# Kernel tuning notes

Measured on AMD Instinct MI355X. Metric: run time of the kernel, lower is better.

The kernel has to match this reference:

```python
import jax, jax.numpy as jnp
import numpy as np

N_NODES = 50000


def setup_inputs() -> dict:
    key = jax.random.key(0)
    k1, k2, k3, k4 = jax.random.split(key, 4)
    x = jax.random.normal(k1, (N_NODES, 256), dtype=jnp.float32)
    edge_index = jax.random.randint(k2, (2, 800000), 0, N_NODES, dtype=jnp.int64)
    W1 = jax.random.normal(k3, (256, 128), dtype=jnp.float32) * (1.0 / np.sqrt(256))
    b1 = jnp.zeros((128,), dtype=jnp.float32)
    W2 = jax.random.normal(k4, (128, 16), dtype=jnp.float32) * (1.0 / np.sqrt(128))
    b2 = jnp.zeros((16,), dtype=jnp.float32)
    return {"x": x, "edge_index": edge_index, "W1": W1, "b1": b1, "W2": W2, "b2": b2}


def _gcn_norm(edge_index, num_nodes):
    # add self-loops, then symmetric normalization D^-1/2 A D^-1/2 (PyG GCNConv default)
    loop = jnp.arange(num_nodes, dtype=edge_index.dtype)
    src = jnp.concatenate([edge_index[0], loop])
    dst = jnp.concatenate([edge_index[1], loop])
    deg = jax.ops.segment_sum(jnp.ones_like(dst, dtype=jnp.float32), dst, num_segments=num_nodes)
    dinv = jnp.where(deg > 0, jax.lax.rsqrt(deg), 0.0)
    norm = dinv[src] * dinv[dst]  # [E+N]
    return src, dst, norm


def _gcn_conv(h, W, b, src, dst, norm, num_nodes):
    h = h @ W                             # linear before propagate
    msg = h[src] * norm[:, None]          # gather + edge scaling
    agg = jax.ops.segment_sum(msg, dst, num_segments=num_nodes)  # scatter-add
    return agg + b


def reference(x, edge_index, W1, b1, W2, b2):
    n = x.shape[0]
    src, dst, norm = _gcn_norm(edge_index, n)
    h = jax.nn.relu(_gcn_conv(x, W1, b1, src, dst, norm, n))
    # F.dropout(training=False) is identity in eval mode
    out = _gcn_conv(h, W2, b2, src, dst, norm, n)
    return jax.nn.log_softmax(out, axis=1)
```

## Files before the change

kernel.cpp:

```cpp
#include <hip/hip_runtime.h>
#include <hip/hip_bf16.h>
#include <math.h>


#define FIN 256
#define FH  128
#define FO  16
#define NCOPY 8

typedef unsigned int uint;
typedef unsigned short ushort;
typedef __attribute__((ext_vector_type(8))) short bf16x8;
typedef __attribute__((ext_vector_type(4))) float f32x4;

static __device__ __forceinline__ ushort f2bf(float f) {
    __hip_bfloat16 b = __float2bfloat16(f);
    return *reinterpret_cast<ushort*>(&b);
}
static __device__ __forceinline__ float bf2f(ushort u) {
    return __uint_as_float(((uint)u) << 16);
}

__global__ __launch_bounds__(256) void GCN_zerowprep_k(int* __restrict__ count8,
                                                       int total8,
                                                       const float* __restrict__ W1,
                                                       ushort* __restrict__ whT,
                                                       ushort* __restrict__ wlT,
                                                       int nZero) {
    if ((int)blockIdx.x < nZero) {
        int i = blockIdx.x * 256 + threadIdx.x;
        if (i < total8) count8[i] = 0;
    } else {
        int i = (blockIdx.x - nZero) * 256 + threadIdx.x;
        int k = i >> 7, c = i & 127;
        float w = W1[i];
        ushort hh = f2bf(w);
        ushort hl = f2bf(w - bf2f(hh));
        whT[c * 256 + k] = hh;
        wlT[c * 256 + k] = hl;
    }
}

#define G1_BR 64
#define G1_KC 32

__global__ __launch_bounds__(256, 4) void GCN_histgemm_k(
        const float* __restrict__ x, const ushort* __restrict__ whT,
        const ushort* __restrict__ wlT, ushort* __restrict__ h1,
        const int* __restrict__ edge, int* __restrict__ count8,
        int* __restrict__ rank, int N, int E, int nGemm) {
    __shared__ __align__(16) ushort xh_s[G1_BR * G1_KC];
    __shared__ __align__(16) ushort xl_s[G1_BR * G1_KC];
    __shared__ __align__(16) ushort wh_s[FH * G1_KC];
    __shared__ __align__(16) ushort wl_s[FH * G1_KC];
    int tid = threadIdx.x;

    if ((int)blockIdx.x >= nGemm) {
        int b = blockIdx.x - nGemm;
        int i = b * 256 + tid;
        if (i < E) {
            int c = b & (NCOPY - 1);
            rank[i] = atomicAdd(&count8[(size_t)c * N + edge[E + i]], 1);
        }
        return;
    }

    int row0 = blockIdx.x * G1_BR;
    int ln = tid & 63;
    int w  = tid >> 6;
    int ln15 = ln & 15;
    int q16  = ln >> 4;

    f32x4 acc[4][2];
    #pragma unroll
    for (int mr = 0; mr < 4; mr++)
        #pragma unroll
        for (int nc = 0; nc < 2; nc++) acc[mr][nc] = (f32x4){0.f, 0.f, 0.f, 0.f};

    for (int kc = 0; kc < FIN; kc += G1_KC) {
        #pragma unroll
        for (int j = 0; j < 2; j++) {
            int u = tid + j * 256;
            int r = u >> 3, kq = u & 7;
            int gr = row0 + r;
            float4 v = make_float4(0.f, 0.f, 0.f, 0.f);
            if (gr < N) v = *(const float4*)&x[(size_t)gr * FIN + kc + kq * 4];
            ushort h0 = f2bf(v.x), h1v = f2bf(v.y), h2 = f2bf(v.z), h3 = f2bf(v.w);
            ushort l0 = f2bf(v.x - bf2f(h0));
            ushort l1 = f2bf(v.y - bf2f(h1v));
            ushort l2 = f2bf(v.z - bf2f(h2));
            ushort l3 = f2bf(v.w - bf2f(h3));
            uint2 hw, lw;
            hw.x = (uint)h0 | ((uint)h1v << 16);
            hw.y = (uint)h2 | ((uint)h3 << 16);
            lw.x = (uint)l0 | ((uint)l1 << 16);
            lw.y = (uint)l2 | ((uint)l3 << 16);
            int byte = (r * 64 + kq * 8) ^ (((r >> 1) & 3) << 4);
            *(uint2*)((char*)xh_s + byte) = hw;
            *(uint2*)((char*)xl_s + byte) = lw;
        }
        #pragma unroll
        for (int j = 0; j < 2; j++) {
            int u = tid + j * 256;
            int c = u >> 2, ku = u & 3;
            uint4 vh = *(const uint4*)&whT[(size_t)c * 256 + kc + ku * 8];
            uint4 vl = *(const uint4*)&wlT[(size_t)c * 256 + kc + ku * 8];
            int byte = (c * 64 + ku * 16) ^ (((c >> 1) & 3) << 4);
            *(uint4*)((char*)wh_s + byte) = vh;
            *(uint4*)((char*)wl_s + byte) = vl;
        }
        __syncthreads();

        bf16x8 ah[4], al[4], bh[2], bl[2];
        #pragma unroll
        for (int mr = 0; mr < 4; mr++) {
            int r = mr * 16 + ln15;
            int byte = r * 64 + ((q16 * 16) ^ (((r >> 1) & 3) << 4));
            ah[mr] = *(const bf16x8*)((const char*)xh_s + byte);
            al[mr] = *(const bf16x8*)((const char*)xl_s + byte);
        }
        #pragma unroll
        for (int nc = 0; nc < 2; nc++) {
            int c = w * 32 + nc * 16 + ln15;
            int byte = c * 64 + ((q16 * 16) ^ (((c >> 1) & 3) << 4));
            bh[nc] = *(const bf16x8*)((const char*)wh_s + byte);
            bl[nc] = *(const bf16x8*)((const char*)wl_s + byte);
        }
        #pragma unroll
        for (int mr = 0; mr < 4; mr++)
            #pragma unroll
            for (int nc = 0; nc < 2; nc++) {
                acc[mr][nc] = __builtin_amdgcn_mfma_f32_16x16x32_bf16(
                    ah[mr], bh[nc], acc[mr][nc], 0, 0, 0);
                acc[mr][nc] = __builtin_amdgcn_mfma_f32_16x16x32_bf16(
                    al[mr], bh[nc], acc[mr][nc], 0, 0, 0);
                acc[mr][nc] = __builtin_amdgcn_mfma_f32_16x16x32_bf16(
                    ah[mr], bl[nc], acc[mr][nc], 0, 0, 0);
            }
        __syncthreads();
    }

    #pragma unroll
    for (int mr = 0; mr < 4; mr++) {
        #pragma unroll
        for (int nc = 0; nc < 2; nc++) {
            int cw = w * 32 + nc * 16 + ln15;
            #pragma unroll
            for (int j = 0; j < 4; j++) {
                int gr = row0 + mr * 16 + q16 * 4 + j;
                if (gr < N) h1[(size_t)gr * FH + cw] = f2bf(acc[mr][nc][j]);
            }
        }
    }
}

__global__ __launch_bounds__(256) void GCN_chpfxbsum_k(int* __restrict__ count8,
                                                       int* __restrict__ count,
                                                       int* __restrict__ bsum,
                                                       int N) {
    int tid = threadIdx.x;
    int d = blockIdx.x * 256 + tid;
    int local = 0;
    if (d < N) {
        int run = 0;
        #pragma unroll
        for (int c = 0; c < NCOPY; c++) {
            int* p = &count8[(size_t)c * N + d];
            int v = *p; *p = run; run += v;
        }
        count[d] = run;
        local = run + 1;
    }
    __shared__ int red[256];
    red[tid] = local;
    __syncthreads();
    for (int st = 128; st > 0; st >>= 1) {
        if (tid < st) red[tid] += red[tid + st];
        __syncthreads();
    }
    if (tid == 0) bsum[blockIdx.x] = red[0];
}

__global__ __launch_bounds__(256) void GCN_scan2_k(const int* __restrict__ count,
                                                   const int* __restrict__ bsum,
                                                   int2* __restrict__ rd2,
                                                   int2* __restrict__ edata, int N) {
    int tid = threadIdx.x;
    int b = blockIdx.x;
    int d = b * 256 + tid;
    int cnt1 = (d < N) ? count[d] + 1 : 0;

    __shared__ int red[256];
    int offp = 0;
    for (int t = tid; t < b; t += 256) offp += bsum[t];
    red[tid] = offp;
    __syncthreads();
    for (int st = 128; st > 0; st >>= 1) {
        if (tid < st) red[tid] += red[tid + st];
        __syncthreads();
    }
    int blockOff = red[0];
    __syncthreads();

    __shared__ int ssum[256];
    ssum[tid] = cnt1;
    __syncthreads();
    for (int off = 1; off < 256; off <<= 1) {
        int t = (tid >= off) ? ssum[tid - off] : 0;
        __syncthreads();
        ssum[tid] += t;
        __syncthreads();
    }
    int r = blockOff + ssum[tid] - cnt1;

    if (d < N) {
        float dv = rsqrtf((float)cnt1);
        rd2[d] = make_int2(r, __float_as_int(dv));
        edata[r] = make_int2(d, __float_as_int(dv * dv));
    }
    if (b == gridDim.x - 1 && tid == 255) rd2[N] = make_int2(blockOff + ssum[255], 0);
}

__global__ __launch_bounds__(256) void GCN_fill_k(const int* __restrict__ edge,
                                                  const int* __restrict__ rank,
                                                  const int* __restrict__ count8,
                                                  const int2* __restrict__ rd2,
                                                  int2* __restrict__ edata,
                                                  int N, int E) {
    int i = blockIdx.x * 256 + threadIdx.x;
    if (i >= E) return;
    int s = edge[i];
    int d = edge[E + i];
    int rk = rank[i];
    int c = (i >> 8) & (NCOPY - 1);
    int2 rdd = rd2[d];
    float ds = __int_as_float(rd2[s].y);
    int slot = rdd.x + 1 + count8[(size_t)c * N + d] + rk;
    edata[slot] = make_int2(s, __float_as_int(ds * __int_as_float(rdd.y)));
}

__global__ __launch_bounds__(256) void GCN_agg1gemm2_k(
        const ushort* __restrict__ h1, const int2* __restrict__ rd2,
        const int2* __restrict__ ed, const float* __restrict__ b1,
        const float* __restrict__ W2, ushort* __restrict__ h2b, int N) {
    __shared__ float w2s[FH][FO];
    __shared__ float hs[16][FH + 4];
    int tid = threadIdx.x;
    #pragma unroll
    for (int j = 0; j < (FH * FO) / 256; j++) {
        int i = tid + j * 256;
        w2s[i >> 4][i & 15] = W2[i];
    }

    int node0 = blockIdx.x * 16;
    int local = tid >> 4;
    int j = tid & 15;
    int node = node0 + local;

    if (node < N) {
        int beg = rd2[node].x, end = rd2[node + 1].x;
        const uint4* hp = (const uint4*)h1;

        float a[8];
        #pragma unroll
        for (int t = 0; t < 8; t++) a[t] = 0.f;

        int i = beg;
        for (; i + 4 <= end; i += 4) {
            int2 e0 = ed[i + 0], e1 = ed[i + 1], e2 = ed[i + 2], e3 = ed[i + 3];
            float w0 = __int_as_float(e0.y), w1 = __int_as_float(e1.y);
            float w2 = __int_as_float(e2.y), w3 = __int_as_float(e3.y);
            uint4 g0 = hp[(size_t)e0.x * 16 + j];
            uint4 g1 = hp[(size_t)e1.x * 16 + j];
            uint4 g2 = hp[(size_t)e2.x * 16 + j];
            uint4 g3 = hp[(size_t)e3.x * 16 + j];
            #pragma unroll
            for (int q = 0; q < 4; q++) {
                uint u0 = (&g0.x)[q], u1 = (&g1.x)[q], u2 = (&g2.x)[q], u3 = (&g3.x)[q];
                a[q*2+0] += __uint_as_float(u0 << 16) * w0;
                a[q*2+1] += __uint_as_float(u0 & 0xFFFF0000u) * w0;
                a[q*2+0] += __uint_as_float(u1 << 16) * w1;
                a[q*2+1] += __uint_as_float(u1 & 0xFFFF0000u) * w1;
                a[q*2+0] += __uint_as_float(u2 << 16) * w2;
                a[q*2+1] += __uint_as_float(u2 & 0xFFFF0000u) * w2;
                a[q*2+0] += __uint_as_float(u3 << 16) * w3;
                a[q*2+1] += __uint_as_float(u3 & 0xFFFF0000u) * w3;
            }
        }
        for (; i < end; i++) {
            int2 e = ed[i];
            float w = __int_as_float(e.y);
            uint4 g = hp[(size_t)e.x * 16 + j];
            #pragma unroll
            for (int q = 0; q < 4; q++) {
                uint u = (&g.x)[q];
                a[q*2+0] += __uint_as_float(u << 16) * w;
                a[q*2+1] += __uint_as_float(u & 0xFFFF0000u) * w;
            }
        }

        const float4* bp = (const float4*)b1;
        float4 bb0 = bp[j * 2 + 0];
        float4 bb1 = bp[j * 2 + 1];
        float4 o0, o1;
        o0.x = fmaxf(a[0] + bb0.x, 0.f);
        o0.y = fmaxf(a[1] + bb0.y, 0.f);
        o0.z = fmaxf(a[2] + bb0.z, 0.f);
        o0.w = fmaxf(a[3] + bb0.w, 0.f);
        o1.x = fmaxf(a[4] + bb1.x, 0.f);
        o1.y = fmaxf(a[5] + bb1.y, 0.f);
        o1.z = fmaxf(a[6] + bb1.z, 0.f);
        o1.w = fmaxf(a[7] + bb1.w, 0.f);
        *(float4*)&hs[local][j * 8 + 0] = o0;
        *(float4*)&hs[local][j * 8 + 4] = o1;
    }
    __syncthreads();

    float acc = 0.f;
    #pragma unroll 8
    for (int k = 0; k < FH; k++) acc += hs[local][k] * w2s[k][j];
    if (node < N) h2b[(size_t)node * FO + j] = f2bf(acc);
}

__global__ __launch_bounds__(256) void GCN_agg2_k(const ushort* __restrict__ h2b,
                                                  const int2* __restrict__ rd2,
                                                  const int2* __restrict__ ed,
                                                  const float* __restrict__ b2,
                                                  float* __restrict__ out, int N) {
    int tid = threadIdx.x;
    int node = blockIdx.x * 32 + (tid >> 3);
    if (node >= N) return;
    int f2 = tid & 7;
    int beg = rd2[node].x, end = rd2[node + 1].x;
    const uint* hp = (const uint*)h2b;
    float a0 = 0.f, a1 = 0.f;
    int i = beg;
    for (; i + 4 <= end; i += 4) {
        int2 e0 = ed[i + 0], e1 = ed[i + 1], e2 = ed[i + 2], e3 = ed[i + 3];
        uint u0 = hp[(size_t)e0.x * 8 + f2];
        uint u1 = hp[(size_t)e1.x * 8 + f2];
        uint u2 = hp[(size_t)e2.x * 8 + f2];
        uint u3 = hp[(size_t)e3.x * 8 + f2];
        float w0 = __int_as_float(e0.y), w1 = __int_as_float(e1.y);
        float w2 = __int_as_float(e2.y), w3 = __int_as_float(e3.y);
        a0 += __uint_as_float(u0 << 16) * w0 + __uint_as_float(u1 << 16) * w1
            + __uint_as_float(u2 << 16) * w2 + __uint_as_float(u3 << 16) * w3;
        a1 += __uint_as_float(u0 & 0xFFFF0000u) * w0 + __uint_as_float(u1 & 0xFFFF0000u) * w1
            + __uint_as_float(u2 & 0xFFFF0000u) * w2 + __uint_as_float(u3 & 0xFFFF0000u) * w3;
    }
    for (; i < end; i++) {
        int2 e = ed[i];
        uint u = hp[(size_t)e.x * 8 + f2];
        float w = __int_as_float(e.y);
        a0 += __uint_as_float(u << 16) * w;
        a1 += __uint_as_float(u & 0xFFFF0000u) * w;
    }
    float2 bb = ((const float2*)b2)[f2];
    float v0 = a0 + bb.x;
    float v1 = a1 + bb.y;
    float mx = fmaxf(v0, v1);
    #pragma unroll
    for (int m = 4; m >= 1; m >>= 1) mx = fmaxf(mx, __shfl_xor(mx, m, 8));
    float s = expf(v0 - mx) + expf(v1 - mx);
    #pragma unroll
    for (int m = 4; m >= 1; m >>= 1) s += __shfl_xor(s, m, 8);
    float ls = logf(s);
    float2 o = make_float2(v0 - mx - ls, v1 - mx - ls);
    ((float2*)out)[(size_t)node * 8 + f2] = o;
}

extern "C" void kernel_launch(void* const* d_in, const int* in_sizes, int n_in,
                              void* d_out, int out_size, void* d_ws, size_t ws_size,
                              hipStream_t stream) {
    (void)n_in; (void)out_size; (void)ws_size;
    const float* x  = (const float*)d_in[0];
    const int*   edp = (const int*)d_in[1];
    const float* W1 = (const float*)d_in[2];
    const float* b1 = (const float*)d_in[3];
    const float* W2 = (const float*)d_in[4];
    const float* b2 = (const float*)d_in[5];
    float* out = (float*)d_out;

    int N = in_sizes[0] / FIN;
    int E = in_sizes[1] / 2;
    int M = E + N;
    int nScanBlocks = (N + 255) / 256;

    char* p = (char*)d_ws;
    auto take = [&](size_t bytes) -> char* {
        char* r = p;
        p += (bytes + 255) & ~(size_t)255;
        return r;
    };
    int*    count  = (int*)take((size_t)N * 4);
    int*    count8 = (int*)take((size_t)NCOPY * N * 4);
    int*    rank   = (int*)take((size_t)E * 4);
    int2*   rd2    = (int2*)take((size_t)(N + 1) * 8);
    int*    bsum   = (int*)take((size_t)nScanBlocks * 4);
    int2*   edata  = (int2*)take((size_t)M * 8);
    ushort* whT    = (ushort*)take((size_t)FH * FIN * 2);
    ushort* wlT    = (ushort*)take((size_t)FH * FIN * 2);
    ushort* h1     = (ushort*)take((size_t)N * FH * 2);
    ushort* h2b    = (ushort*)take((size_t)N * FO * 2);

    int eBlocks = (E + 255) / 256;
    int nGemm   = (N + G1_BR - 1) / G1_BR;
    int total8  = NCOPY * N;
    int nZero   = (total8 + 255) / 256;

    GCN_zerowprep_k<<<nZero + (FIN * FH) / 256, 256, 0, stream>>>(
        count8, total8, W1, whT, wlT, nZero);
    GCN_histgemm_k<<<nGemm + eBlocks, 256, 0, stream>>>(
        x, whT, wlT, h1, edp, count8, rank, N, E, nGemm);
    GCN_chpfxbsum_k<<<nScanBlocks, 256, 0, stream>>>(count8, count, bsum, N);
    GCN_scan2_k<<<nScanBlocks, 256, 0, stream>>>(count, bsum, rd2, edata, N);
    GCN_fill_k<<<eBlocks, 256, 0, stream>>>(edp, rank, count8, rd2, edata, N, E);
    GCN_agg1gemm2_k<<<(N + 15) / 16, 256, 0, stream>>>(h1, rd2, edata, b1, W2, h2b, N);
    GCN_agg2_k<<<(N + 31) / 32, 256, 0, stream>>>(h2b, rd2, edata, b2, out, N);
}
```

Before: 120.6 us.

## Replace global-atomic degree histogram with LDS-privatized packed 16-bit chunk histograms

Replaces the 8-copy global atomic degree histogram with per-chunk histograms built in shared memory. Each of 64 edge chunks is handled by 2 blocks that each cover half the nodes, with two 16-bit counters packed per word. This removes global atomics and the zeroing pass, and the histogram becomes its own kernel separate from the GEMM. In exchange it adds a 64-way per-word prefix pass, only 128 histogram blocks, no overlap with the GEMM, and counters that overflow if any node gets more than 65535 edges in one chunk.

New measurement: 130.6 us. 1.08x slower.

```diff
diff --git a/kernel.cpp b/kernel.cpp
--- a/kernel.cpp
+++ b/kernel.cpp
@@ -6,7 +6,8 @@
 #define FIN 256
 #define FH  128
 #define FO  16
-#define NCOPY 8
+#define NCHUNK64 64
+#define WPR_MAX 12544
 
 typedef unsigned int uint;
 typedef unsigned short ushort;
@@ -21,49 +22,60 @@
     return __uint_as_float(((uint)u) << 16);
 }
 
-__global__ __launch_bounds__(256) void GCN_zerowprep_k(int* __restrict__ count8,
-                                                       int total8,
-                                                       const float* __restrict__ W1,
-                                                       ushort* __restrict__ whT,
-                                                       ushort* __restrict__ wlT,
-                                                       int nZero) {
-    if ((int)blockIdx.x < nZero) {
-        int i = blockIdx.x * 256 + threadIdx.x;
-        if (i < total8) count8[i] = 0;
-    } else {
-        int i = (blockIdx.x - nZero) * 256 + threadIdx.x;
-        int k = i >> 7, c = i & 127;
-        float w = W1[i];
-        ushort hh = f2bf(w);
-        ushort hl = f2bf(w - bf2f(hh));
-        whT[c * 256 + k] = hh;
-        wlT[c * 256 + k] = hl;
-    }
+__global__ __launch_bounds__(256) void GCN_wprep_k(const float* __restrict__ W1,
+                                                   ushort* __restrict__ whT,
+                                                   ushort* __restrict__ wlT) {
+    int i = blockIdx.x * 256 + threadIdx.x;
+    int k = i >> 7, c = i & 127;
+    float w = W1[i];
+    ushort hh = f2bf(w);
+    ushort hl = f2bf(w - bf2f(hh));
+    whT[c * 256 + k] = hh;
+    wlT[c * 256 + k] = hl;
+}
+
+__global__ __launch_bounds__(256) void GCN_hist_k(const int* __restrict__ edge,
+                                                  uint* __restrict__ cw,
+                                                  int* __restrict__ rank,
+                                                  int E, int ech,
+                                                  int nWords, int wpr) {
+    __shared__ uint lh[WPR_MAX];
+    int tid = threadIdx.x;
+    int r = blockIdx.x & 1;
+    int c = blockIdx.x >> 1;
+    int w0 = r * wpr;
+    int wlim = nWords - w0; if (wlim > wpr) wlim = wpr;
+    for (int j = tid; j < wlim; j += 256) lh[j] = 0;
+    __syncthreads();
+    int base = c * ech;
+    int lim = base + ech; if (lim > E) lim = E;
+    for (int i = base + tid; i < lim; i += 256) {
+        int d = edge[E + i];
+        int wd = (d >> 1) - w0;
+        if ((unsigned)wd < (unsigned)wlim) {
+            int sh = (d & 1) << 4;
+            uint old = atomicAdd(&lh[wd], 1u << sh);
+            rank[i] = (int)((old >> sh) & 0xFFFFu);
+        }
+    }
+    __syncthreads();
+    for (int j = tid; j < wlim; j += 256)
+        cw[(size_t)c * nWords + w0 + j] = lh[j];
 }
 
 #define G1_BR 64
 #define G1_KC 32
 
-__global__ __launch_bounds__(256, 4) void GCN_histgemm_k(
-        const float* __restrict__ x, const ushort* __restrict__ whT,
-        const ushort* __restrict__ wlT, ushort* __restrict__ h1,
-        const int* __restrict__ edge, int* __restrict__ count8,
-        int* __restrict__ rank, int N, int E, int nGemm) {
+__global__ __launch_bounds__(256, 4) void GCN_gemm1_k(const float* __restrict__ x,
+                                                      const ushort* __restrict__ whT,
+                                                      const ushort* __restrict__ wlT,
+                                                      ushort* __restrict__ h1,
+                                                      int N) {
     __shared__ __align__(16) ushort xh_s[G1_BR * G1_KC];
     __shared__ __align__(16) ushort xl_s[G1_BR * G1_KC];
     __shared__ __align__(16) ushort wh_s[FH * G1_KC];
     __shared__ __align__(16) ushort wl_s[FH * G1_KC];
     int tid = threadIdx.x;
-
-    if ((int)blockIdx.x >= nGemm) {
-        int b = blockIdx.x - nGemm;
-        int i = b * 256 + tid;
-        if (i < E) {
-            int c = b & (NCOPY - 1);
-            rank[i] = atomicAdd(&count8[(size_t)c * N + edge[E + i]], 1);
-        }
-        return;
-    }
 
     int row0 = blockIdx.x * G1_BR;
     int ln = tid & 63;
@@ -144,41 +156,46 @@
     for (int mr = 0; mr < 4; mr++) {
         #pragma unroll
         for (int nc = 0; nc < 2; nc++) {
-            int cw = w * 32 + nc * 16 + ln15;
+            int cw2 = w * 32 + nc * 16 + ln15;
             #pragma unroll
             for (int j = 0; j < 4; j++) {
                 int gr = row0 + mr * 16 + q16 * 4 + j;
-                if (gr < N) h1[(size_t)gr * FH + cw] = f2bf(acc[mr][nc][j]);
+                if (gr < N) h1[(size_t)gr * FH + cw2] = f2bf(acc[mr][nc][j]);
             }
         }
     }
 }
 
-__global__ __launch_bounds__(256) void GCN_chpfxbsum_k(int* __restrict__ count8,
-                                                       int* __restrict__ count,
-                                                       int* __restrict__ bsum,
-                                                       int N) {
-    int tid = threadIdx.x;
-    int d = blockIdx.x * 256 + tid;
+__global__ __launch_bounds__(256) void GCN_chpfx_k(uint* __restrict__ cw,
+                                                   int* __restrict__ count,
+                                                   int* __restrict__ bsum,
+                                                   int N, int nWords) {
+    int tid = threadIdx.x;
+    int w = blockIdx.x * 256 + tid;
     int local = 0;
-    if (d < N) {
-        int run = 0;
-        #pragma unroll
-        for (int c = 0; c < NCOPY; c++) {
-            int* p = &count8[(size_t)c * N + d];
-            int v = *p; *p = run; run += v;
-        }
-        count[d] = run;
-        local = run + 1;
+    if (w < nWords) {
+        uint re = 0, ro = 0;
+        #pragma unroll 8
+        for (int c = 0; c < NCHUNK64; c++) {
+            uint* p = &cw[(size_t)c * nWords + w];
+            uint v = *p;
+            *p = re | (ro << 16);
+            re += v & 0xFFFFu;
+            ro += v >> 16;
+        }
+        int d0 = 2 * w;
+        if (d0 < N)     { count[d0]     = (int)re; local += (int)re + 1; }
+        if (d0 + 1 < N) { count[d0 + 1] = (int)ro; local += (int)ro + 1; }
     }
     __shared__ int red[256];
     red[tid] = local;
     __syncthreads();
-    for (int st = 128; st > 0; st >>= 1) {
-        if (tid < st) red[tid] += red[tid + st];
-        __syncthreads();
-    }
-    if (tid == 0) bsum[blockIdx.x] = red[0];
+    for (int st = 64; st > 0; st >>= 1) {
+        if ((tid & 127) < st) red[tid] += red[tid + st];
+        __syncthreads();
+    }
+    if (tid == 0)   bsum[blockIdx.x * 2 + 0] = red[0];
+    if (tid == 128) bsum[blockIdx.x * 2 + 1] = red[128];
 }
 
 __global__ __launch_bounds__(256) void GCN_scan2_k(const int* __restrict__ count,
@@ -223,20 +240,22 @@
 
 __global__ __launch_bounds__(256) void GCN_fill_k(const int* __restrict__ edge,
                                                   const int* __restrict__ rank,
-                                                  const int* __restrict__ count8,
+                                                  const uint* __restrict__ cw,
                                                   const int2* __restrict__ rd2,
                                                   int2* __restrict__ edata,
-                                                  int N, int E) {
+                                                  int E, int ech, int nWords) {
     int i = blockIdx.x * 256 + threadIdx.x;
     if (i >= E) return;
     int s = edge[i];
     int d = edge[E + i];
     int rk = rank[i];
-    int c = (i >> 8) & (NCOPY - 1);
+    int c = i / ech;
+    uint pw = cw[(size_t)c * nWords + (d >> 1)];
+    int pfx = (int)((pw >> ((d & 1) << 4)) & 0xFFFFu);
     int2 rdd = rd2[d];
     float ds = __int_as_float(rd2[s].y);
-    int slot = rdd.x + 1 + count8[(size_t)c * N + d] + rk;
-    edata[slot] = make_int2(s, __float_as_int(ds * __int_as_float(rdd.y)));
+    edata[rdd.x + 1 + pfx + rk] =
+        make_int2(s, __float_as_int(ds * __int_as_float(rdd.y)));
 }
 
 __global__ __launch_bounds__(256) void GCN_agg1gemm2_k(
@@ -384,7 +403,11 @@
     int N = in_sizes[0] / FIN;
     int E = in_sizes[1] / 2;
     int M = E + N;
+    int nWords = (N + 1) / 2;
+    int wpr = (nWords + 1) / 2;
+    int ech = (E + NCHUNK64 - 1) / NCHUNK64;
     int nScanBlocks = (N + 255) / 256;
+    int nChpfx = (nWords + 255) / 256;
 
     char* p = (char*)d_ws;
     auto take = [&](size_t bytes) -> char* {
@@ -393,10 +416,10 @@
         return r;
     };
     int*    count  = (int*)take((size_t)N * 4);
-    int*    count8 = (int*)take((size_t)NCOPY * N * 4);
     int*    rank   = (int*)take((size_t)E * 4);
+    uint*   cw     = (uint*)take((size_t)NCHUNK64 * nWords * 4);
     int2*   rd2    = (int2*)take((size_t)(N + 1) * 8);
-    int*    bsum   = (int*)take((size_t)nScanBlocks * 4);
+    int*    bsum   = (int*)take((size_t)(2 * nChpfx) * 4);
     int2*   edata  = (int2*)take((size_t)M * 8);
     ushort* whT    = (ushort*)take((size_t)FH * FIN * 2);
     ushort* wlT    = (ushort*)take((size_t)FH * FIN * 2);
@@ -405,16 +428,13 @@
 
     int eBlocks = (E + 255) / 256;
     int nGemm   = (N + G1_BR - 1) / G1_BR;
-    int total8  = NCOPY * N;
-    int nZero   = (total8 + 255) / 256;
-
-    GCN_zerowprep_k<<<nZero + (FIN * FH) / 256, 256, 0, stream>>>(
-        count8, total8, W1, whT, wlT, nZero);
-    GCN_histgemm_k<<<nGemm + eBlocks, 256, 0, stream>>>(
-        x, whT, wlT, h1, edp, count8, rank, N, E, nGemm);
-    GCN_chpfxbsum_k<<<nScanBlocks, 256, 0, stream>>>(count8, count, bsum, N);
+
+    GCN_wprep_k<<<(FIN * FH) / 256, 256, 0, stream>>>(W1, whT, wlT);
+    GCN_hist_k<<<2 * NCHUNK64, 256, 0, stream>>>(edp, cw, rank, E, ech, nWords, wpr);
+    GCN_gemm1_k<<<nGemm, 256, 0, stream>>>(x, whT, wlT, h1, N);
+    GCN_chpfx_k<<<nChpfx, 256, 0, stream>>>(cw, count, bsum, N, nWords);
     GCN_scan2_k<<<nScanBlocks, 256, 0, stream>>>(count, bsum, rd2, edata, N);
-    GCN_fill_k<<<eBlocks, 256, 0, stream>>>(edp, rank, count8, rd2, edata, N, E);
+    GCN_fill_k<<<eBlocks, 256, 0, stream>>>(edp, rank, cw, rd2, edata, E, ech, nWords);
     GCN_agg1gemm2_k<<<(N + 15) / 16, 256, 0, stream>>>(h1, rd2, edata, b1, W2, h2b, N);
     GCN_agg2_k<<<(N + 31) / 32, 256, 0, stream>>>(h2b, rd2, edata, b2, out, N);
 }
```
